# Performance work log

Hardware: AMD Instinct MI355X
Metric: run time of the kernel (lower is better)

Reference implementation:

```python
import jax, jax.numpy as jnp
import numpy as np

K = 2            # top-k experts per sample
LOSS_COEF = 0.01


def _cv_squared(v):
    eps = 1e-10
    return jnp.var(v, ddof=1) / (jnp.mean(v) ** 2 + eps)


def setup_inputs() -> dict:
    key = jax.random.key(0)
    k1, k2, k3, k4 = jax.random.split(key, 4)
    B, S, D, O, E = 32, 512, 768, 768, 8
    return {
        "x": jax.random.normal(k1, (B, S, D), dtype=jnp.float32),
        "w_gate": jax.random.normal(k2, (D, E), dtype=jnp.float32) * 0.02,
        "weight": jax.random.normal(k3, (E, O, D), dtype=jnp.float32) * 0.02,
        "bias": jax.random.normal(k4, (E, O), dtype=jnp.float32) * 0.02,
    }


def reference(x, w_gate, weight, bias):
    # x: [B, S, D]; w_gate: [D, E]; weight: [E, O, D]; bias: [E, O]
    B = x.shape[0]
    E = w_gate.shape[1]

    # --- top-k gating (eval mode: clean logits, no noise) ---
    pooled = x.mean(-2)                       # [B, D] (moe_level != 'task'/'token')
    logits = pooled @ w_gate                  # [B, E]
    top_vals, top_idx = jax.lax.top_k(logits, min(K + 1, E))
    tk_vals, tk_idx = top_vals[:, :K], top_idx[:, :K]
    tk_gates = jax.nn.softmax(tk_vals, axis=1)            # [B, K]
    gates = jnp.zeros_like(logits).at[jnp.arange(B)[:, None], tk_idx].set(tk_gates)  # [B, E]

    load = (gates > 0).sum(0).astype(jnp.float32)          # [E]
    importance = gates.sum(0)                              # [E]
    loss = (_cv_squared(importance) + _cv_squared(load)) * LOSS_COEF

    # --- per-sample soft combination of expert weights, then batched linear ---
    # same math as sum_e gates[b,e] * weight[e] without materializing [B,E,O,D]
    expert_w = jnp.einsum('be,eoi->boi', gates, weight)    # [B, O, D]
    expert_b = jnp.einsum('be,eo->bo', gates, bias)        # [B, O]
    y = jnp.einsum('bij,bkj->bik', x, expert_w) + expert_b[:, None, :]  # [B, S, O]
    return (y, loss)
```

## Files before the change

kernel.cpp:

```cpp
#include <hip/hip_runtime.h>
#include <hip/hip_bf16.h>
#include <stdint.h>

#define B_ 32
#define S_ 512
#define D_ 768
#define O_ 768
#define E_ 8
#define YSIZE (B_ * S_ * O_)
#define BK 32
#define WSLICE (O_ * D_)

typedef __attribute__((ext_vector_type(8))) short bf16x8;
typedef __attribute__((ext_vector_type(4))) float f32x4;

static __device__ __forceinline__ unsigned short f2bf(float f) {
  union { float f; uint32_t u; } v; v.f = f;
  uint32_t u = v.u;
  uint32_t r = u + 0x7fff + ((u >> 16) & 1);
  return (unsigned short)(r >> 16);
}

static __device__ __forceinline__ void async_load16(const void* g, void* l) {
  __builtin_amdgcn_global_load_lds(
      (const __attribute__((address_space(1))) void*)g,
      (__attribute__((address_space(3))) void*)l, 16, 0, 0);
}

__global__ __launch_bounds__(192) void k_pool_convert(
    const float* __restrict__ x, unsigned short* __restrict__ xb,
    float* __restrict__ psum) {
  int t  = threadIdx.x;
  int b  = blockIdx.x;
  int sc = blockIdx.y;
  size_t rowbase = (size_t)(b * S_ + sc * 32) * D_;
  const float* xp = x + rowbase + 4 * t;
  unsigned short* op = xb + rowbase + 4 * t;
  float4 sum = {0.f, 0.f, 0.f, 0.f};
  #pragma unroll 8
  for (int s = 0; s < 32; ++s) {
    float4 v = *(const float4*)(xp + (size_t)s * D_);
    sum.x += v.x; sum.y += v.y; sum.z += v.z; sum.w += v.w;
    ushort4 o;
    o.x = f2bf(v.x); o.y = f2bf(v.y); o.z = f2bf(v.z); o.w = f2bf(v.w);
    *(ushort4*)(op + (size_t)s * D_) = o;
  }
  *(float4*)(psum + (size_t)(sc * B_ + b) * D_ + 4 * t) = sum;
}

__global__ __launch_bounds__(256) void k_logits(
    const float* __restrict__ psum, const float* __restrict__ w_gate,
    float* __restrict__ gates, int* __restrict__ eidx,
    float* __restrict__ gval) {
  int b = blockIdx.x;
  int tid = threadIdx.x;
  float acc[E_];
  #pragma unroll
  for (int e = 0; e < E_; ++e) acc[e] = 0.f;

  for (int d = tid; d < D_; d += 256) {
    float p = 0.f;
    #pragma unroll
    for (int c = 0; c < 16; ++c) p += psum[(c * B_ + b) * D_ + d];
    p *= (1.0f / (float)S_);
    const float* wg = w_gate + d * E_;
    #pragma unroll
    for (int e = 0; e < E_; ++e) acc[e] += p * wg[e];
  }
  #pragma unroll
  for (int off = 32; off > 0; off >>= 1) {
    #pragma unroll
    for (int e = 0; e < E_; ++e) acc[e] += __shfl_down(acc[e], off, 64);
  }
  __shared__ float part[4][E_];
  if ((tid & 63) == 0) {
    #pragma unroll
    for (int e = 0; e < E_; ++e) part[tid >> 6][e] = acc[e];
  }
  __syncthreads();
  if (tid == 0) {
    float lg[E_];
    #pragma unroll
    for (int e = 0; e < E_; ++e)
      lg[e] = part[0][e] + part[1][e] + part[2][e] + part[3][e];
    int i0 = 0; float v0 = lg[0];
    #pragma unroll
    for (int e = 1; e < E_; ++e) { if (lg[e] > v0) { v0 = lg[e]; i0 = e; } }
    int i1 = -1; float v1 = -1e30f;
    #pragma unroll
    for (int e = 0; e < E_; ++e) {
      if (e == i0) continue;
      if (lg[e] > v1) { v1 = lg[e]; i1 = e; }
    }
    float m  = fmaxf(v0, v1);
    float x0 = expf(v0 - m), x1 = expf(v1 - m);
    float s  = x0 + x1;
    float g0 = x0 / s, g1 = x1 / s;
    #pragma unroll
    for (int e = 0; e < E_; ++e)
      gates[b * E_ + e] = (e == i0) ? g0 : ((e == i1) ? g1 : 0.f);
    eidx[b] = i0; eidx[B_ + b] = i1;
    gval[b] = g0; gval[B_ + b] = g1;
  }
}

__global__ __launch_bounds__(256) void k_combine(
    const float* __restrict__ weight, const float* __restrict__ gates,
    unsigned short* __restrict__ wc, float* __restrict__ loss_out) {
  __shared__ float gsh[B_][E_];
  int tid = threadIdx.x;
  if (tid < B_ * E_) ((float*)gsh)[tid] = gates[tid];
  __syncthreads();

  if (blockIdx.x == 0 && blockIdx.y == 0 && tid == 0) {
    double mi = 0, ml = 0;
    float imp[E_], ldv[E_];
    #pragma unroll
    for (int e = 0; e < E_; ++e) {
      float s = 0.f, c = 0.f;
      for (int b = 0; b < B_; ++b) {
        float g = gsh[b][e];
        s += g; c += (g > 0.f) ? 1.f : 0.f;
      }
      imp[e] = s; ldv[e] = c;
      mi += s; ml += c;
    }
    mi /= E_; ml /= E_;
    double vi = 0, vl = 0;
    #pragma unroll
    for (int e = 0; e < E_; ++e) {
      double di = imp[e] - mi, dl = ldv[e] - ml;
      vi += di * di; vl += dl * dl;
    }
    vi /= (E_ - 1); vl /= (E_ - 1);
    loss_out[0] = (float)((vi / (mi * mi + 1e-10) + vl / (ml * ml + 1e-10)) * 0.01);
  }

  size_t i = (size_t)blockIdx.x * 2048 + tid * 8;
  int b0 = blockIdx.y * 8;
  float v[E_][8];
  #pragma unroll
  for (int e = 0; e < E_; ++e) {
    float4 u0 = *(const float4*)(weight + (size_t)e * WSLICE + i);
    float4 u1 = *(const float4*)(weight + (size_t)e * WSLICE + i + 4);
    v[e][0] = u0.x; v[e][1] = u0.y; v[e][2] = u0.z; v[e][3] = u0.w;
    v[e][4] = u1.x; v[e][5] = u1.y; v[e][6] = u1.z; v[e][7] = u1.w;
  }
  #pragma unroll
  for (int bb = 0; bb < 8; ++bb) {
    int b = b0 + bb;
    float c[8];
    #pragma unroll
    for (int j = 0; j < 8; ++j) c[j] = 0.f;
    #pragma unroll
    for (int e = 0; e < E_; ++e) {
      float g = gsh[b][e];
      #pragma unroll
      for (int j = 0; j < 8; ++j) c[j] += g * v[e][j];
    }
    uint32_t pk[4];
    #pragma unroll
    for (int j = 0; j < 4; ++j)
      pk[j] = (uint32_t)f2bf(c[2 * j]) | ((uint32_t)f2bf(c[2 * j + 1]) << 16);
    *(uint4*)(wc + (size_t)b * WSLICE + i) = make_uint4(pk[0], pk[1], pk[2], pk[3]);
  }
}

__global__ __launch_bounds__(256) void k_moe_gemm(
    const unsigned short* __restrict__ xb, const unsigned short* __restrict__ wc,
    const int* __restrict__ eidx, const float* __restrict__ gval,
    const float* __restrict__ bias, float* __restrict__ y) {
  __shared__ unsigned short Alds[128 * BK];
  __shared__ unsigned short Blds[128 * BK];

  int b    = blockIdx.y;
  int tile = blockIdx.x;
  int st = tile & 3;
  int ot = tile >> 2;
  int s0 = st * 128, o0 = ot * 128;

  int tid  = threadIdx.x;
  int wave = tid >> 6, lane = tid & 63;
  int wm = wave & 1, wn = wave >> 1;

  const unsigned short* Abase = xb + ((size_t)(b * S_ + s0)) * D_;
  const unsigned short* Bbase = wc + (size_t)b * WSLICE + (size_t)o0 * D_;

  f32x4 acc[4][4];
  #pragma unroll
  for (int i = 0; i < 4; ++i)
    #pragma unroll
    for (int j = 0; j < 4; ++j) acc[i][j] = (f32x4){0.f, 0.f, 0.f, 0.f};

  int a_chunk0 = wave * 2;
  int a_r = lane >> 2;
  int a_c = (lane & 3) * 8;

  for (int kk = 0; kk < D_; kk += BK) {
    __syncthreads();
    #pragma unroll
    for (int j = 0; j < 2; ++j) {
      int chunk = a_chunk0 + j;
      const unsigned short* srcA =
          Abase + (size_t)(chunk * 16 + a_r) * D_ + kk + a_c;
      async_load16(srcA, Alds + chunk * 512);
      const unsigned short* srcB =
          Bbase + (size_t)(chunk * 16 + a_r) * D_ + kk + a_c;
      async_load16(srcB, Blds + chunk * 512);
    }
    __syncthreads();

    bf16x8 af[4], bfr[4];
    int koff = (lane >> 4) * 8;
    int r16  = lane & 15;
    #pragma unroll
    for (int mi = 0; mi < 4; ++mi)
      af[mi] = *(const bf16x8*)(Alds + (wm * 64 + mi * 16 + r16) * BK + koff);
    #pragma unroll
    for (int ni = 0; ni < 4; ++ni)
      bfr[ni] = *(const bf16x8*)(Blds + (wn * 64 + ni * 16 + r16) * BK + koff);
    #pragma unroll
    for (int mi = 0; mi < 4; ++mi)
      #pragma unroll
      for (int ni = 0; ni < 4; ++ni)
        acc[mi][ni] = __builtin_amdgcn_mfma_f32_16x16x32_bf16(
            af[mi], bfr[ni], acc[mi][ni], 0, 0, 0);
  }

  int   e0 = eidx[b], e1 = eidx[B_ + b];
  float g0 = gval[b], g1 = gval[B_ + b];
  float* Y = y + ((size_t)(b * S_ + s0)) * O_ + o0;
  int col   = lane & 15;
  int rquad = (lane >> 4) * 4;
  #pragma unroll
  for (int ni = 0; ni < 4; ++ni) {
    int n = wn * 64 + ni * 16 + col;
    float cbv = g0 * bias[e0 * O_ + o0 + n] + g1 * bias[e1 * O_ + o0 + n];
    #pragma unroll
    for (int mi = 0; mi < 4; ++mi) {
      #pragma unroll
      for (int r = 0; r < 4; ++r) {
        int m = wm * 64 + mi * 16 + rquad + r;
        Y[(size_t)m * O_ + n] = acc[mi][ni][r] + cbv;
      }
    }
  }
}

extern "C" void kernel_launch(void* const* d_in, const int* in_sizes, int n_in,
                              void* d_out, int out_size, void* d_ws, size_t ws_size,
                              hipStream_t stream) {
  const float* x      = (const float*)d_in[0];
  const float* w_gate = (const float*)d_in[1];
  const float* weight = (const float*)d_in[2];
  const float* bias   = (const float*)d_in[3];
  float* y = (float*)d_out;

  float* psum  = (float*)d_ws;
  float* gates = (float*)((char*)d_ws + 1572864);
  int*   eidx  = (int*)((char*)d_ws + 1573888);
  float* gval  = (float*)((char*)d_ws + 1574144);
  unsigned short* xb = (unsigned short*)((char*)d_ws + 2097152);
  unsigned short* wc = (unsigned short*)((char*)d_ws + 27262976);

  k_pool_convert<<<dim3(32, 16), 192, 0, stream>>>(x, xb, psum);
  k_logits<<<32, 256, 0, stream>>>(psum, w_gate, gates, eidx, gval);
  k_combine<<<dim3(288, 4), 256, 0, stream>>>(weight, gates, wc, y + YSIZE);
  k_moe_gemm<<<dim3(24, 32), 256, 0, stream>>>(xb, wc, eidx, gval, bias, y);
}
```

Baseline: 171.9 us.

## Double K-step per barrier and remap GEMM blocks to XCDs by batch

The GEMM now loads two BK slices per synchronization, which halves the number of barrier pairs and issues more async loads per round trip. The launch grid is flattened and blocks are remapped so each batch's tiles land on the same XCD, meant to improve L2 reuse of that batch's combined weights and activations. It also adds a launch_bounds occupancy hint of 3. LDS use doubles, and the loads are still not overlapped with compute, so latency hiding depends on occupancy.

```diff
diff --git a/kernel.cpp b/kernel.cpp
--- a/kernel.cpp
+++ b/kernel.cpp
@@ -166,15 +166,18 @@
   }
 }
 
-__global__ __launch_bounds__(256) void k_moe_gemm(
+__global__ __launch_bounds__(256, 3) void k_moe_gemm(
     const unsigned short* __restrict__ xb, const unsigned short* __restrict__ wc,
     const int* __restrict__ eidx, const float* __restrict__ gval,
     const float* __restrict__ bias, float* __restrict__ y) {
-  __shared__ unsigned short Alds[128 * BK];
-  __shared__ unsigned short Blds[128 * BK];
-
-  int b    = blockIdx.y;
-  int tile = blockIdx.x;
+  __shared__ unsigned short Alds[2][128 * BK];
+  __shared__ unsigned short Blds[2][128 * BK];
+
+  int flat = blockIdx.x;
+  int xcd  = flat & 7;
+  int slot = flat >> 3;
+  int b    = xcd + 8 * (slot / 24);
+  int tile = slot % 24;
   int st = tile & 3;
   int ot = tile >> 2;
   int s0 = st * 128, o0 = ot * 128;
@@ -196,35 +199,41 @@
   int a_r = lane >> 2;
   int a_c = (lane & 3) * 8;
 
-  for (int kk = 0; kk < D_; kk += BK) {
+  for (int kk = 0; kk < D_; kk += 2 * BK) {
     __syncthreads();
     #pragma unroll
-    for (int j = 0; j < 2; ++j) {
-      int chunk = a_chunk0 + j;
-      const unsigned short* srcA =
-          Abase + (size_t)(chunk * 16 + a_r) * D_ + kk + a_c;
-      async_load16(srcA, Alds + chunk * 512);
-      const unsigned short* srcB =
-          Bbase + (size_t)(chunk * 16 + a_r) * D_ + kk + a_c;
-      async_load16(srcB, Blds + chunk * 512);
+    for (int sl = 0; sl < 2; ++sl) {
+      #pragma unroll
+      for (int j = 0; j < 2; ++j) {
+        int chunk = a_chunk0 + j;
+        const unsigned short* srcA =
+            Abase + (size_t)(chunk * 16 + a_r) * D_ + kk + sl * BK + a_c;
+        async_load16(srcA, &Alds[sl][chunk * 512]);
+        const unsigned short* srcB =
+            Bbase + (size_t)(chunk * 16 + a_r) * D_ + kk + sl * BK + a_c;
+        async_load16(srcB, &Blds[sl][chunk * 512]);
+      }
     }
     __syncthreads();
 
-    bf16x8 af[4], bfr[4];
     int koff = (lane >> 4) * 8;
     int r16  = lane & 15;
     #pragma unroll
-    for (int mi = 0; mi < 4; ++mi)
-      af[mi] = *(const bf16x8*)(Alds + (wm * 64 + mi * 16 + r16) * BK + koff);
-    #pragma unroll
-    for (int ni = 0; ni < 4; ++ni)
-      bfr[ni] = *(const bf16x8*)(Blds + (wn * 64 + ni * 16 + r16) * BK + koff);
-    #pragma unroll
-    for (int mi = 0; mi < 4; ++mi)
+    for (int sl = 0; sl < 2; ++sl) {
+      bf16x8 af[4], bfr[4];
+      #pragma unroll
+      for (int mi = 0; mi < 4; ++mi)
+        af[mi] = *(const bf16x8*)(&Alds[sl][(wm * 64 + mi * 16 + r16) * BK + koff]);
       #pragma unroll
       for (int ni = 0; ni < 4; ++ni)
-        acc[mi][ni] = __builtin_amdgcn_mfma_f32_16x16x32_bf16(
-            af[mi], bfr[ni], acc[mi][ni], 0, 0, 0);
+        bfr[ni] = *(const bf16x8*)(&Blds[sl][(wn * 64 + ni * 16 + r16) * BK + koff]);
+      #pragma unroll
+      for (int mi = 0; mi < 4; ++mi)
+        #pragma unroll
+        for (int ni = 0; ni < 4; ++ni)
+          acc[mi][ni] = __builtin_amdgcn_mfma_f32_16x16x32_bf16(
+              af[mi], bfr[ni], acc[mi][ni], 0, 0, 0);
+    }
   }
 
   int   e0 = eidx[b], e1 = eidx[B_ + b];
@@ -266,5 +275,5 @@
   k_pool_convert<<<dim3(32, 16), 192, 0, stream>>>(x, xb, psum);
   k_logits<<<32, 256, 0, stream>>>(psum, w_gate, gates, eidx, gval);
   k_combine<<<dim3(288, 4), 256, 0, stream>>>(weight, gates, wc, y + YSIZE);
-  k_moe_gemm<<<dim3(24, 32), 256, 0, stream>>>(xb, wc, eidx, gval, bias, y);
-}
+  k_moe_gemm<<<768, 256, 0, stream>>>(xb, wc, eidx, gval, bias, y);
+}
```

After: 161.8 us. 5.8% less time.
